# Performance work log

Hardware: AMD Instinct MI355X
Metric: run time of the kernel (lower is better)

Reference implementation:

```python
import jax, jax.numpy as jnp
import numpy as np

N_HEADS = 16


def setup_inputs() -> dict:
    key = jax.random.key(0)
    k1, k2, k3 = jax.random.split(key, 3)
    B, T, D = 2, 2048, 1024
    x = jax.random.normal(k1, (B, T, D), dtype=jnp.float32)
    w_qkv = jax.random.normal(k2, (3 * D, D), dtype=jnp.float32) * 0.02
    w_proj = jax.random.normal(k3, (D, D), dtype=jnp.float32) * (0.02 / np.sqrt(24.0))
    return {"x": x, "w_qkv": w_qkv, "w_proj": w_proj}


def reference(x, w_qkv, w_proj):
    B, T, D = x.shape
    H = N_HEADS
    dh = D // H
    # qkv linear (no bias): x @ w_qkv.T -> [B, T, 3D]
    qkv = jnp.einsum('btd,ed->bte', x, w_qkv)
    q, k, v = jnp.split(qkv, 3, axis=-1)
    q = q.reshape(B, T, H, dh)
    k = k.reshape(B, T, H, dh)
    v = v.reshape(B, T, H, dh)
    # attention with materialized scores [B, H, T, S]
    scores = jnp.einsum('bthd,bshd->bhts', q, k) / jnp.sqrt(jnp.asarray(dh, x.dtype))
    attn = jax.nn.softmax(scores.astype(jnp.float32), axis=-1).astype(x.dtype)
    out = jnp.einsum('bhts,bshd->bthd', attn, v).reshape(B, T, D)
    # output projection (no bias)
    return jnp.einsum('btd,ed->bte', out, w_proj)
```

## Files before the change

kernel.cpp:

```cpp
#include <hip/hip_runtime.h>


typedef __attribute__((ext_vector_type(8))) short s8v;
typedef __attribute__((ext_vector_type(8))) unsigned short us8;
typedef __attribute__((ext_vector_type(4))) unsigned short us4;
typedef __attribute__((ext_vector_type(4))) float f4v;
typedef __attribute__((ext_vector_type(16))) float f16v;
typedef __attribute__((ext_vector_type(4))) unsigned u4v;

__device__ __forceinline__ unsigned short f2b(float f) {
    unsigned u = __builtin_bit_cast(unsigned, f);
    u += 0x7FFFu + ((u >> 16) & 1u);
    return (unsigned short)(u >> 16);
}
__device__ __forceinline__ unsigned packtrunc(float a, float b, unsigned sel) {
    unsigned r;
    asm("v_perm_b32 %0, %1, %2, %3"
        : "=v"(r)
        : "v"(__builtin_bit_cast(unsigned, b)), "v"(__builtin_bit_cast(unsigned, a)), "s"(sel));
    return r;
}

#if __has_builtin(__builtin_amdgcn_exp2f)
#define EXP2F(x) __builtin_amdgcn_exp2f(x)
#else
#define EXP2F(x) exp2f(x)
#endif

#define QSCALE 0.18033688011112042f

__global__ __launch_bounds__(256) void cvt_all(const float* __restrict__ x,
                                               const float* __restrict__ wq,
                                               const float* __restrict__ wp,
                                               unsigned short* __restrict__ xb,
                                               unsigned short* __restrict__ wqb,
                                               unsigned short* __restrict__ wpb) {
    const int nx = 4096 * 1024 / 4, nq = 3072 * 1024 / 4;
    int i = blockIdx.x * 256 + threadIdx.x;
    const float* s;
    unsigned short* d;
    int j;
    if (i < nx)           { s = x;  d = xb;  j = i; }
    else if (i < nx + nq) { s = wq; d = wqb; j = i - nx; }
    else                  { s = wp; d = wpb; j = i - nx - nq; }
    float4 v = ((const float4*)s)[j];
    ushort4 o;
    o.x = f2b(v.x); o.y = f2b(v.y); o.z = f2b(v.z); o.w = f2b(v.w);
    ((ushort4*)d)[j] = o;
}

#define GLD_LDS16(g, l)                                                                        \
    __builtin_amdgcn_global_load_lds((const __attribute__((address_space(1))) unsigned*)(g),   \
                                     (__attribute__((address_space(3))) unsigned*)(l), 16, 0, 0)

__global__ __launch_bounds__(256, 4) void gemm_qkv(const unsigned short* __restrict__ A,
                                                   const unsigned short* __restrict__ B,
                                                   unsigned short* __restrict__ qkvb) {
    __shared__ unsigned short As[128][64];
    __shared__ unsigned short Bs[128][64];
    const int tid = threadIdx.x;
    const int l = tid & 63, w = tid >> 6;
    const int quad = l >> 4, ln = l & 15;
    const int m0 = blockIdx.y * 128, n0 = blockIdx.x * 128;
    const int wm = (w >> 1) * 64, wn = (w & 1) * 64;

    const f4v fz = {0.f, 0.f, 0.f, 0.f};
    f4v acc[4][4];
#pragma unroll
    for (int i = 0; i < 4; ++i)
#pragma unroll
        for (int j = 0; j < 4; ++j) acc[i][j] = fz;

    const int srow = tid >> 3, sc8 = tid & 7;
    const int gcol = ((sc8 ^ (srow & 7)) << 3);
    const int koff0 = ((quad ^ (ln & 7)) << 3);
    const int koff1 = (((4 + quad) ^ (ln & 7)) << 3);

    const unsigned short* pa = A + (size_t)(m0 + srow) * 1024 + gcol;
    const unsigned short* pb = B + (size_t)(n0 + srow) * 1024 + gcol;

    for (int k0 = 0; k0 < 1024; k0 += 64) {
#pragma unroll
        for (int b = 0; b < 4; ++b) {
            GLD_LDS16(pa + (size_t)32 * b * 1024 + k0, &As[srow + 32 * b][sc8 * 8]);
            GLD_LDS16(pb + (size_t)32 * b * 1024 + k0, &Bs[srow + 32 * b][sc8 * 8]);
        }
        __syncthreads();
#pragma unroll
        for (int ks = 0; ks < 2; ++ks) {
            const int ko = ks ? koff1 : koff0;
            s8v af[4], bf[4];
#pragma unroll
            for (int mt = 0; mt < 4; ++mt) af[mt] = *(const s8v*)&As[wm + mt * 16 + ln][ko];
#pragma unroll
            for (int nt = 0; nt < 4; ++nt) bf[nt] = *(const s8v*)&Bs[wn + nt * 16 + ln][ko];
#pragma unroll
            for (int mt = 0; mt < 4; ++mt)
#pragma unroll
                for (int nt = 0; nt < 4; ++nt)
                    acc[mt][nt] = __builtin_amdgcn_mfma_f32_16x16x32_bf16(af[mt], bf[nt], acc[mt][nt], 0, 0, 0);
        }
        __syncthreads();
    }

#pragma unroll
    for (int mt = 0; mt < 4; ++mt)
#pragma unroll
        for (int nt = 0; nt < 4; ++nt) {
            const int col = n0 + wn + nt * 16 + ln;
            const int row = m0 + wm + mt * 16 + quad * 4;
            const float sc = (col < 1024) ? QSCALE : 1.0f;
#pragma unroll
            for (int r = 0; r < 4; ++r)
                qkvb[(size_t)(row + r) * 3072 + col] = f2b(acc[mt][nt][r] * sc);
        }
}

__global__ __launch_bounds__(256, 4) void gemm_proj(const unsigned short* __restrict__ A,
                                                    const unsigned short* __restrict__ B,
                                                    float* __restrict__ C) {
    __shared__ unsigned short As[64][64];
    __shared__ unsigned short Bs[64][64];
    const int tid = threadIdx.x;
    const int l = tid & 63, w = tid >> 6;
    const int quad = l >> 4, ln = l & 15;
    const int m0 = blockIdx.y * 64, n0 = blockIdx.x * 64;
    const int wm = (w >> 1) * 32, wn = (w & 1) * 32;

    const f4v fz = {0.f, 0.f, 0.f, 0.f};
    f4v acc[2][2];
#pragma unroll
    for (int i = 0; i < 2; ++i)
#pragma unroll
        for (int j = 0; j < 2; ++j) acc[i][j] = fz;

    const int srow = tid >> 3, sc8 = tid & 7;
    const int gcol = ((sc8 ^ (srow & 7)) << 3);
    const int koff0 = ((quad ^ (ln & 7)) << 3);
    const int koff1 = (((4 + quad) ^ (ln & 7)) << 3);

    for (int k0 = 0; k0 < 1024; k0 += 64) {
#pragma unroll
        for (int b = 0; b < 2; ++b) {
            GLD_LDS16(A + (size_t)(m0 + srow + 32 * b) * 1024 + k0 + gcol, &As[srow + 32 * b][sc8 * 8]);
            GLD_LDS16(B + (size_t)(n0 + srow + 32 * b) * 1024 + k0 + gcol, &Bs[srow + 32 * b][sc8 * 8]);
        }
        __syncthreads();
#pragma unroll
        for (int ks = 0; ks < 2; ++ks) {
            const int ko = ks ? koff1 : koff0;
            s8v af[2], bf[2];
#pragma unroll
            for (int mt = 0; mt < 2; ++mt) af[mt] = *(const s8v*)&As[wm + mt * 16 + ln][ko];
#pragma unroll
            for (int nt = 0; nt < 2; ++nt) bf[nt] = *(const s8v*)&Bs[wn + nt * 16 + ln][ko];
#pragma unroll
            for (int mt = 0; mt < 2; ++mt)
#pragma unroll
                for (int nt = 0; nt < 2; ++nt)
                    acc[mt][nt] = __builtin_amdgcn_mfma_f32_16x16x32_bf16(af[mt], bf[nt], acc[mt][nt], 0, 0, 0);
        }
        __syncthreads();
    }

#pragma unroll
    for (int mt = 0; mt < 2; ++mt)
#pragma unroll
        for (int nt = 0; nt < 2; ++nt) {
            const int row = m0 + wm + mt * 16 + quad * 4;
            const int col = n0 + wn + nt * 16 + ln;
#pragma unroll
            for (int r = 0; r < 4; ++r) C[(size_t)(row + r) * 1024 + col] = acc[mt][nt][r];
        }
}

__global__ __launch_bounds__(256, 4) void attn_split(const unsigned short* __restrict__ qkvb,
                                                     float* __restrict__ opart,
                                                     float* __restrict__ lpart) {
    __shared__ unsigned short Ks[2][64][76];
    __shared__ unsigned short Vt[2][64][76];

    const int tid = threadIdx.x;
    const int l = tid & 63, w = tid >> 6;
    const int m31 = l & 31, h2 = l >> 5;
    const int qw = w * 32;
    const int t0 = blockIdx.x * 128;
    const int hh = blockIdx.y;
    const int bb = blockIdx.z >> 1, sp = blockIdx.z & 1;
    const size_t rowbase = (size_t)bb * 2048;
    const int sbase = sp * 1024;
    const unsigned sel = 0x07060302u;

#pragma unroll
    for (int it = 0; it < 4; ++it) {
        const int idx = tid + it * 256;
        const int qr = idx >> 3, qc = (idx & 7) * 8;
        unsigned short* dst = (qr < 64) ? &Ks[0][qr][qc] : &Ks[1][qr - 64][qc];
        *(us8*)dst = *(const us8*)(qkvb + (rowbase + t0 + qr) * 3072 + hh * 64 + qc);
    }
    __syncthreads();
    s8v qf[4];
    {
        const int qrow = qw + m31;
#pragma unroll
        for (int k4 = 0; k4 < 4; ++k4)
            qf[k4] = (qrow < 64) ? *(const s8v*)&Ks[0][qrow][k4 * 16 + h2 * 8]
                                 : *(const s8v*)&Ks[1][qrow - 64][k4 * 16 + h2 * 8];
    }
    __syncthreads();

    const int r0 = tid >> 3, c0 = (tid & 7) * 8;
    const int va = tid >> 4, vc = tid & 15;

    f16v zz;
#pragma unroll
    for (int i = 0; i < 16; ++i) zz[i] = 0.f;
    f16v oacc[2];
    oacc[0] = zz; oacc[1] = zz;
    float lsum = 0.f;

    us8 kreg0 = *(const us8*)(qkvb + (rowbase + sbase + r0) * 3072 + 1024 + hh * 64 + c0);
    us8 kreg1 = *(const us8*)(qkvb + (rowbase + sbase + r0 + 32) * 3072 + 1024 + hh * 64 + c0);
    us4 vreg[4];
#pragma unroll
    for (int j = 0; j < 4; ++j)
        vreg[j] = *(const us4*)(qkvb + (rowbase + sbase + 4 * va + j) * 3072 + 2048 + hh * 64 + 4 * vc);
    *(us8*)&Ks[0][r0][c0] = kreg0;
    *(us8*)&Ks[0][r0 + 32][c0] = kreg1;
#pragma unroll
    for (int dd = 0; dd < 4; ++dd) {
        unsigned lo = (unsigned)vreg[0][dd] | ((unsigned)vreg[1][dd] << 16);
        unsigned hi = (unsigned)vreg[2][dd] | ((unsigned)vreg[3][dd] << 16);
        uint2 pk2; pk2.x = lo; pk2.y = hi;
        *(uint2*)&Vt[0][4 * vc + dd][4 * va] = pk2;
    }

    for (int i = 0; i < 16; ++i) {
        const int cur = i & 1;
        __syncthreads();

        if (i + 1 < 16) {
            const size_t sn = rowbase + sbase + (i + 1) * 64;
            kreg0 = *(const us8*)(qkvb + (sn + r0) * 3072 + 1024 + hh * 64 + c0);
            kreg1 = *(const us8*)(qkvb + (sn + r0 + 32) * 3072 + 1024 + hh * 64 + c0);
#pragma unroll
            for (int j = 0; j < 4; ++j)
                vreg[j] = *(const us4*)(qkvb + (sn + 4 * va + j) * 3072 + 2048 + hh * 64 + 4 * vc);
        }

#pragma unroll
        for (int st = 0; st < 2; ++st) {
            f16v sacc = zz;
            __builtin_amdgcn_s_setprio(1);
#pragma unroll
            for (int k4 = 0; k4 < 4; ++k4) {
                s8v kf = *(const s8v*)&Ks[cur][st * 32 + m31][k4 * 16 + h2 * 8];
                sacc = __builtin_amdgcn_mfma_f32_32x32x16_bf16(kf, qf[k4], sacc, 0, 0, 0);
            }
            __builtin_amdgcn_s_setprio(0);
            unsigned wv[4][2];
#pragma unroll
            for (int g = 0; g < 4; ++g) {
                float p0 = EXP2F(sacc[g * 4 + 0]);
                float p1 = EXP2F(sacc[g * 4 + 1]);
                float p2 = EXP2F(sacc[g * 4 + 2]);
                float p3 = EXP2F(sacc[g * 4 + 3]);
                lsum += (p0 + p1) + (p2 + p3);
                wv[g][0] = packtrunc(p0, p1, sel);
                wv[g][1] = packtrunc(p2, p3, sel);
            }
            __builtin_amdgcn_s_setprio(1);
#pragma unroll
            for (int e = 0; e < 2; ++e) {
                auto ra = __builtin_amdgcn_permlane32_swap(wv[2 * e][0], wv[2 * e + 1][0], false, false);
                auto rb = __builtin_amdgcn_permlane32_swap(wv[2 * e][1], wv[2 * e + 1][1], false, false);
                u4v t;
                t[0] = ra[0]; t[1] = rb[0];
                t[2] = ra[1]; t[3] = rb[1];
                s8v pf = __builtin_bit_cast(s8v, t);
                const int k2 = 2 * st + e;
#pragma unroll
                for (int nt = 0; nt < 2; ++nt) {
                    s8v vfr = *(const s8v*)&Vt[cur][nt * 32 + m31][k2 * 16 + h2 * 8];
                    oacc[nt] = __builtin_amdgcn_mfma_f32_32x32x16_bf16(pf, vfr, oacc[nt], 0, 0, 0);
                }
            }
            __builtin_amdgcn_s_setprio(0);
        }

        if (i + 1 < 16) {
            *(us8*)&Ks[1 - cur][r0][c0] = kreg0;
            *(us8*)&Ks[1 - cur][r0 + 32][c0] = kreg1;
#pragma unroll
            for (int dd = 0; dd < 4; ++dd) {
                unsigned lo = (unsigned)vreg[0][dd] | ((unsigned)vreg[1][dd] << 16);
                unsigned hi = (unsigned)vreg[2][dd] | ((unsigned)vreg[3][dd] << 16);
                uint2 pk2; pk2.x = lo; pk2.y = hi;
                *(uint2*)&Vt[1 - cur][4 * vc + dd][4 * va] = pk2;
            }
        }
    }

    lsum += __shfl_xor(lsum, 32, 64);
    if (h2 == 0)
        lpart[((size_t)sp * 4096 + rowbase + t0 + qw + m31) * 16 + hh] = lsum;

    float* op = opart + (size_t)sp * 4096 * 1024;
#pragma unroll
    for (int nt = 0; nt < 2; ++nt)
#pragma unroll
        for (int g = 0; g < 4; ++g)
#pragma unroll
            for (int r = 0; r < 4; ++r) {
                const int qrow = 8 * g + 4 * h2 + r;
                op[(rowbase + t0 + qw + qrow) * 1024 + hh * 64 + nt * 32 + m31] = oacc[nt][g * 4 + r];
            }
}

__global__ __launch_bounds__(256) void attn_combine(const float* __restrict__ opart,
                                                    const float* __restrict__ lpart,
                                                    unsigned short* __restrict__ attnb) {
    const int idx = blockIdx.x * 256 + threadIdx.x;
    const int r = idx >> 8, c4 = (idx & 255) << 2, h = c4 >> 6;
    const size_t fi = (size_t)r * 256 + (c4 >> 2);
    float4 o0 = ((const float4*)opart)[fi];
    float4 o1 = ((const float4*)(opart + (size_t)4096 * 1024))[fi];
    float ls = lpart[(size_t)r * 16 + h] + lpart[((size_t)4096 + r) * 16 + h];
    float s = 1.001955f / ls;
    ushort4 o;
    o.x = f2b((o0.x + o1.x) * s);
    o.y = f2b((o0.y + o1.y) * s);
    o.z = f2b((o0.z + o1.z) * s);
    o.w = f2b((o0.w + o1.w) * s);
    ((ushort4*)attnb)[fi] = o;
}

__global__ __launch_bounds__(256) void attn_mfma(const unsigned short* __restrict__ qkvb,
                                                 unsigned short* __restrict__ attnb) {
    __shared__ unsigned short Ks[2][64][76];
    __shared__ unsigned short Vt[2][64][76];
    __shared__ float lred[128];

    const int tid = threadIdx.x;
    const int l = tid & 63, w = tid >> 6;
    const int m31 = l & 31, h2 = l >> 5;
    const int qw = w * 32;
    const int t0 = blockIdx.x * 128;
    const int hh = blockIdx.y, bb = blockIdx.z;
    const size_t rowbase = (size_t)bb * 2048;
    const unsigned sel = 0x07060302u;

#pragma unroll
    for (int it = 0; it < 4; ++it) {
        const int idx = tid + it * 256;
        const int qr = idx >> 3, qc = (idx & 7) * 8;
        unsigned short* dst = (qr < 64) ? &Ks[0][qr][qc] : &Ks[1][qr - 64][qc];
        *(us8*)dst = *(const us8*)(qkvb + (rowbase + t0 + qr) * 3072 + hh * 64 + qc);
    }
    __syncthreads();
    s8v qf[4];
    {
        const int qrow = qw + m31;
#pragma unroll
        for (int k4 = 0; k4 < 4; ++k4)
            qf[k4] = (qrow < 64) ? *(const s8v*)&Ks[0][qrow][k4 * 16 + h2 * 8]
                                 : *(const s8v*)&Ks[1][qrow - 64][k4 * 16 + h2 * 8];
    }
    __syncthreads();

    const int r0 = tid >> 3, c0 = (tid & 7) * 8;
    const int va = tid >> 4, vc = tid & 15;

    f16v zz;
#pragma unroll
    for (int i = 0; i < 16; ++i) zz[i] = 0.f;
    f16v oacc[2];
    oacc[0] = zz; oacc[1] = zz;
    float lsum = 0.f;

    us8 kreg0 = *(const us8*)(qkvb + (rowbase + r0) * 3072 + 1024 + hh * 64 + c0);
    us8 kreg1 = *(const us8*)(qkvb + (rowbase + r0 + 32) * 3072 + 1024 + hh * 64 + c0);
    us4 vreg[4];
#pragma unroll
    for (int j = 0; j < 4; ++j)
        vreg[j] = *(const us4*)(qkvb + (rowbase + 4 * va + j) * 3072 + 2048 + hh * 64 + 4 * vc);
    *(us8*)&Ks[0][r0][c0] = kreg0;
    *(us8*)&Ks[0][r0 + 32][c0] = kreg1;
#pragma unroll
    for (int dd = 0; dd < 4; ++dd) {
        unsigned lo = (unsigned)vreg[0][dd] | ((unsigned)vreg[1][dd] << 16);
        unsigned hi = (unsigned)vreg[2][dd] | ((unsigned)vreg[3][dd] << 16);
        uint2 pk2; pk2.x = lo; pk2.y = hi;
        *(uint2*)&Vt[0][4 * vc + dd][4 * va] = pk2;
    }

    for (int i = 0; i < 32; ++i) {
        const int cur = i & 1;
        __syncthreads();

        if (i + 1 < 32) {
            const int sn = (i + 1) * 64;
            kreg0 = *(const us8*)(qkvb + (rowbase + sn + r0) * 3072 + 1024 + hh * 64 + c0);
            kreg1 = *(const us8*)(qkvb + (rowbase + sn + r0 + 32) * 3072 + 1024 + hh * 64 + c0);
#pragma unroll
            for (int j = 0; j < 4; ++j)
                vreg[j] = *(const us4*)(qkvb + (rowbase + sn + 4 * va + j) * 3072 + 2048 + hh * 64 + 4 * vc);
        }

        f16v sacc[2];
        sacc[0] = zz; sacc[1] = zz;
#pragma unroll
        for (int k4 = 0; k4 < 4; ++k4) {
#pragma unroll
            for (int st = 0; st < 2; ++st) {
                s8v kf = *(const s8v*)&Ks[cur][st * 32 + m31][k4 * 16 + h2 * 8];
                sacc[st] = __builtin_amdgcn_mfma_f32_32x32x16_bf16(kf, qf[k4], sacc[st], 0, 0, 0);
            }
        }

        unsigned wv[2][4][2];
#pragma unroll
        for (int st = 0; st < 2; ++st)
#pragma unroll
            for (int g = 0; g < 4; ++g) {
                float p0 = EXP2F(sacc[st][g * 4 + 0]);
                float p1 = EXP2F(sacc[st][g * 4 + 1]);
                float p2 = EXP2F(sacc[st][g * 4 + 2]);
                float p3 = EXP2F(sacc[st][g * 4 + 3]);
                lsum += (p0 + p1) + (p2 + p3);
                wv[st][g][0] = packtrunc(p0, p1, sel);
                wv[st][g][1] = packtrunc(p2, p3, sel);
            }

        s8v pf[4];
#pragma unroll
        for (int st = 0; st < 2; ++st)
#pragma unroll
            for (int e = 0; e < 2; ++e) {
                auto ra = __builtin_amdgcn_permlane32_swap(wv[st][2 * e][0], wv[st][2 * e + 1][0], false, false);
                auto rb = __builtin_amdgcn_permlane32_swap(wv[st][2 * e][1], wv[st][2 * e + 1][1], false, false);
                u4v t;
                t[0] = ra[0]; t[1] = rb[0];
                t[2] = ra[1]; t[3] = rb[1];
                pf[2 * st + e] = __builtin_bit_cast(s8v, t);
            }

#pragma unroll
        for (int k2 = 0; k2 < 4; ++k2) {
#pragma unroll
            for (int nt = 0; nt < 2; ++nt) {
                s8v vfr = *(const s8v*)&Vt[cur][nt * 32 + m31][k2 * 16 + h2 * 8];
                oacc[nt] = __builtin_amdgcn_mfma_f32_32x32x16_bf16(pf[k2], vfr, oacc[nt], 0, 0, 0);
            }
        }

        if (i + 1 < 32) {
            *(us8*)&Ks[1 - cur][r0][c0] = kreg0;
            *(us8*)&Ks[1 - cur][r0 + 32][c0] = kreg1;
#pragma unroll
            for (int dd = 0; dd < 4; ++dd) {
                unsigned lo = (unsigned)vreg[0][dd] | ((unsigned)vreg[1][dd] << 16);
                unsigned hi = (unsigned)vreg[2][dd] | ((unsigned)vreg[3][dd] << 16);
                uint2 pk2; pk2.x = lo; pk2.y = hi;
                *(uint2*)&Vt[1 - cur][4 * vc + dd][4 * va] = pk2;
            }
        }
    }

    lsum += __shfl_xor(lsum, 32, 64);
    lred[qw + m31] = lsum;
    float inv[16];
#pragma unroll
    for (int g = 0; g < 4; ++g)
#pragma unroll
        for (int r = 0; r < 4; ++r)
            inv[g * 4 + r] = 1.001955f / lred[qw + 8 * g + 4 * h2 + r];

#pragma unroll
    for (int nt = 0; nt < 2; ++nt)
#pragma unroll
        for (int g = 0; g < 4; ++g)
#pragma unroll
            for (int r = 0; r < 4; ++r) {
                const int qrow = 8 * g + 4 * h2 + r;
                float o = oacc[nt][g * 4 + r] * inv[g * 4 + r];
                attnb[(rowbase + t0 + qw + qrow) * 1024 + hh * 64 + nt * 32 + m31] = f2b(o);
            }
}

extern "C" void kernel_launch(void* const* d_in, const int* in_sizes, int n_in,
                              void* d_out, int out_size, void* d_ws, size_t ws_size,
                              hipStream_t stream) {
    const float* x      = (const float*)d_in[0];
    const float* w_qkv  = (const float*)d_in[1];
    const float* w_proj = (const float*)d_in[2];
    float* out = (float*)d_out;

    char* p = (char*)d_ws;
    unsigned short* xb    = (unsigned short*)p;  p += (size_t)4096 * 1024 * 2;
    unsigned short* wqb   = (unsigned short*)p;  p += (size_t)3072 * 1024 * 2;
    unsigned short* wpb   = (unsigned short*)p;  p += (size_t)1024 * 1024 * 2;
    unsigned short* qkvb  = (unsigned short*)p;  p += (size_t)4096 * 3072 * 2;
    unsigned short* attnb = (unsigned short*)p;  p += (size_t)4096 * 1024 * 2;
    float* opart = (float*)p;  p += (size_t)2 * 4096 * 1024 * 4;
    float* lpart = (float*)p;  p += (size_t)2 * 4096 * 16 * 4;
    const size_t need = (size_t)(p - (char*)d_ws);

    cvt_all<<<8192, 256, 0, stream>>>(x, w_qkv, w_proj, xb, wqb, wpb);

    gemm_qkv<<<dim3(3072 / 128, 4096 / 128), 256, 0, stream>>>(xb, wqb, qkvb);

    if (ws_size >= need) {
        attn_split<<<dim3(2048 / 128, 16, 4), 256, 0, stream>>>(qkvb, opart, lpart);
        attn_combine<<<4096, 256, 0, stream>>>(opart, lpart, attnb);
    } else {
        attn_mfma<<<dim3(2048 / 128, 16, 2), 256, 0, stream>>>(qkvb, attnb);
    }

    gemm_proj<<<dim3(1024 / 64, 4096 / 64), 256, 0, stream>>>(attnb, wpb, out);
}
```

Baseline: 176.8 us.

## Fuse all stages into one cooperative persistent kernel with grid syncs

Replaces the five separate launches (convert, QKV GEMM, split attention, combine, projection GEMM) with a single cooperative kernel of 1024 blocks that runs each stage in turn, separated by grid.sync(). The aim is to remove per-launch overhead and the idle gaps between kernels. The cost is grid-wide barriers and fixed block-to-work mappings: the QKV GEMM uses only 768 of the 1024 blocks, and every stage is limited to 1024 resident blocks. The cooperative path is taken only when the stream is not being captured, and the old multi-kernel path remains as a fallback.

```diff
diff --git a/kernel.cpp b/kernel.cpp
--- a/kernel.cpp
+++ b/kernel.cpp
@@ -1,4 +1,7 @@
 #include <hip/hip_runtime.h>
+#include <hip/hip_cooperative_groups.h>
+
+namespace cg = cooperative_groups;
 
 
 typedef __attribute__((ext_vector_type(8))) short s8v;
@@ -28,6 +31,325 @@
 #endif
 
 #define QSCALE 0.18033688011112042f
+
+#define GLD_LDS16(g, l)                                                                        \
+    __builtin_amdgcn_global_load_lds((const __attribute__((address_space(1))) unsigned*)(g),   \
+                                     (__attribute__((address_space(3))) unsigned*)(l), 16, 0, 0)
+
+typedef unsigned short row64_t[64];
+typedef unsigned short kvbuf_t[64][76];
+
+__global__ __launch_bounds__(256, 4) void mha_mega(const float* __restrict__ x,
+                                                   const float* __restrict__ wq,
+                                                   const float* __restrict__ wp,
+                                                   unsigned short* __restrict__ xb,
+                                                   unsigned short* __restrict__ wqb,
+                                                   unsigned short* __restrict__ wpb,
+                                                   unsigned short* __restrict__ qkvb,
+                                                   float* __restrict__ opart,
+                                                   float* __restrict__ lpart,
+                                                   float* __restrict__ out) {
+    __shared__ __align__(16) unsigned char smem[38912];
+    const int tid = threadIdx.x;
+    const int bid = blockIdx.x;
+    cg::grid_group grid = cg::this_grid();
+
+    {
+        const int nx = 4096 * 1024 / 4, nq = 3072 * 1024 / 4;
+#pragma unroll
+        for (int it = 0; it < 8; ++it) {
+            const int i = it * 262144 + bid * 256 + tid;
+            const float* s;
+            unsigned short* d;
+            int j;
+            if (i < nx)           { s = x;  d = xb;  j = i; }
+            else if (i < nx + nq) { s = wq; d = wqb; j = i - nx; }
+            else                  { s = wp; d = wpb; j = i - nx - nq; }
+            float4 v = ((const float4*)s)[j];
+            ushort4 o;
+            o.x = f2b(v.x); o.y = f2b(v.y); o.z = f2b(v.z); o.w = f2b(v.w);
+            ((ushort4*)d)[j] = o;
+        }
+    }
+    grid.sync();
+
+    if (bid < 768) {
+        row64_t* As = (row64_t*)smem;
+        row64_t* Bs = (row64_t*)(smem + 128 * 64 * 2);
+        const int l = tid & 63, w = tid >> 6;
+        const int quad = l >> 4, ln = l & 15;
+        const int m0 = (bid / 24) * 128, n0 = (bid % 24) * 128;
+        const int wm = (w >> 1) * 64, wn = (w & 1) * 64;
+
+        const f4v fz = {0.f, 0.f, 0.f, 0.f};
+        f4v acc[4][4];
+#pragma unroll
+        for (int i = 0; i < 4; ++i)
+#pragma unroll
+            for (int j = 0; j < 4; ++j) acc[i][j] = fz;
+
+        const int srow = tid >> 3, sc8 = tid & 7;
+        const int gcol = ((sc8 ^ (srow & 7)) << 3);
+        const int koff0 = ((quad ^ (ln & 7)) << 3);
+        const int koff1 = (((4 + quad) ^ (ln & 7)) << 3);
+
+        const unsigned short* pa = xb + (size_t)(m0 + srow) * 1024 + gcol;
+        const unsigned short* pb = wqb + (size_t)(n0 + srow) * 1024 + gcol;
+
+        for (int k0 = 0; k0 < 1024; k0 += 64) {
+#pragma unroll
+            for (int b = 0; b < 4; ++b) {
+                GLD_LDS16(pa + (size_t)32 * b * 1024 + k0, &As[srow + 32 * b][sc8 * 8]);
+                GLD_LDS16(pb + (size_t)32 * b * 1024 + k0, &Bs[srow + 32 * b][sc8 * 8]);
+            }
+            __syncthreads();
+#pragma unroll
+            for (int ks = 0; ks < 2; ++ks) {
+                const int ko = ks ? koff1 : koff0;
+                s8v af[4], bf[4];
+#pragma unroll
+                for (int mt = 0; mt < 4; ++mt) af[mt] = *(const s8v*)&As[wm + mt * 16 + ln][ko];
+#pragma unroll
+                for (int nt = 0; nt < 4; ++nt) bf[nt] = *(const s8v*)&Bs[wn + nt * 16 + ln][ko];
+#pragma unroll
+                for (int mt = 0; mt < 4; ++mt)
+#pragma unroll
+                    for (int nt = 0; nt < 4; ++nt)
+                        acc[mt][nt] = __builtin_amdgcn_mfma_f32_16x16x32_bf16(af[mt], bf[nt], acc[mt][nt], 0, 0, 0);
+            }
+            __syncthreads();
+        }
+
+#pragma unroll
+        for (int mt = 0; mt < 4; ++mt)
+#pragma unroll
+            for (int nt = 0; nt < 4; ++nt) {
+                const int col = n0 + wn + nt * 16 + ln;
+                const int row = m0 + wm + mt * 16 + quad * 4;
+                const float sc = (col < 1024) ? QSCALE : 1.0f;
+#pragma unroll
+                for (int r = 0; r < 4; ++r)
+                    qkvb[(size_t)(row + r) * 3072 + col] = f2b(acc[mt][nt][r] * sc);
+            }
+    }
+    grid.sync();
+
+    {
+        kvbuf_t* Ks = (kvbuf_t*)smem;
+        kvbuf_t* Vt = (kvbuf_t*)(smem + 2 * sizeof(kvbuf_t));
+        const int l = tid & 63, w = tid >> 6;
+        const int m31 = l & 31, h2 = l >> 5;
+        const int qw = w * 32;
+        const int t0 = (bid & 15) * 128;
+        const int hh = (bid >> 4) & 15;
+        const int spz = bid >> 8;
+        const int bb = spz >> 1, sp = spz & 1;
+        const size_t rowbase = (size_t)bb * 2048;
+        const int sbase = sp * 1024;
+        const unsigned sel = 0x07060302u;
+
+#pragma unroll
+        for (int it = 0; it < 4; ++it) {
+            const int idx = tid + it * 256;
+            const int qr = idx >> 3, qc = (idx & 7) * 8;
+            unsigned short* dst = (qr < 64) ? &Ks[0][qr][qc] : &Ks[1][qr - 64][qc];
+            *(us8*)dst = *(const us8*)(qkvb + (rowbase + t0 + qr) * 3072 + hh * 64 + qc);
+        }
+        __syncthreads();
+        s8v qf[4];
+        {
+            const int qrow = qw + m31;
+#pragma unroll
+            for (int k4 = 0; k4 < 4; ++k4)
+                qf[k4] = (qrow < 64) ? *(const s8v*)&Ks[0][qrow][k4 * 16 + h2 * 8]
+                                     : *(const s8v*)&Ks[1][qrow - 64][k4 * 16 + h2 * 8];
+        }
+        __syncthreads();
+
+        const int r0 = tid >> 3, c0 = (tid & 7) * 8;
+        const int va = tid >> 4, vc = tid & 15;
+
+        f16v zz;
+#pragma unroll
+        for (int i = 0; i < 16; ++i) zz[i] = 0.f;
+        f16v oacc[2];
+        oacc[0] = zz; oacc[1] = zz;
+        float lsum = 0.f;
+
+        us8 kreg0 = *(const us8*)(qkvb + (rowbase + sbase + r0) * 3072 + 1024 + hh * 64 + c0);
+        us8 kreg1 = *(const us8*)(qkvb + (rowbase + sbase + r0 + 32) * 3072 + 1024 + hh * 64 + c0);
+        us4 vreg[4];
+#pragma unroll
+        for (int j = 0; j < 4; ++j)
+            vreg[j] = *(const us4*)(qkvb + (rowbase + sbase + 4 * va + j) * 3072 + 2048 + hh * 64 + 4 * vc);
+        *(us8*)&Ks[0][r0][c0] = kreg0;
+        *(us8*)&Ks[0][r0 + 32][c0] = kreg1;
+#pragma unroll
+        for (int dd = 0; dd < 4; ++dd) {
+            unsigned lo = (unsigned)vreg[0][dd] | ((unsigned)vreg[1][dd] << 16);
+            unsigned hi = (unsigned)vreg[2][dd] | ((unsigned)vreg[3][dd] << 16);
+            uint2 pk2; pk2.x = lo; pk2.y = hi;
+            *(uint2*)&Vt[0][4 * vc + dd][4 * va] = pk2;
+        }
+
+        for (int i = 0; i < 16; ++i) {
+            const int cur = i & 1;
+            __syncthreads();
+
+            if (i + 1 < 16) {
+                const size_t sn = rowbase + sbase + (i + 1) * 64;
+                kreg0 = *(const us8*)(qkvb + (sn + r0) * 3072 + 1024 + hh * 64 + c0);
+                kreg1 = *(const us8*)(qkvb + (sn + r0 + 32) * 3072 + 1024 + hh * 64 + c0);
+#pragma unroll
+                for (int j = 0; j < 4; ++j)
+                    vreg[j] = *(const us4*)(qkvb + (sn + 4 * va + j) * 3072 + 2048 + hh * 64 + 4 * vc);
+            }
+
+#pragma unroll
+            for (int st = 0; st < 2; ++st) {
+                f16v sacc = zz;
+                __builtin_amdgcn_s_setprio(1);
+#pragma unroll
+                for (int k4 = 0; k4 < 4; ++k4) {
+                    s8v kf = *(const s8v*)&Ks[cur][st * 32 + m31][k4 * 16 + h2 * 8];
+                    sacc = __builtin_amdgcn_mfma_f32_32x32x16_bf16(kf, qf[k4], sacc, 0, 0, 0);
+                }
+                __builtin_amdgcn_s_setprio(0);
+                unsigned wv[4][2];
+#pragma unroll
+                for (int g = 0; g < 4; ++g) {
+                    float p0 = EXP2F(sacc[g * 4 + 0]);
+                    float p1 = EXP2F(sacc[g * 4 + 1]);
+                    float p2 = EXP2F(sacc[g * 4 + 2]);
+                    float p3 = EXP2F(sacc[g * 4 + 3]);
+                    lsum += (p0 + p1) + (p2 + p3);
+                    wv[g][0] = packtrunc(p0, p1, sel);
+                    wv[g][1] = packtrunc(p2, p3, sel);
+                }
+                __builtin_amdgcn_s_setprio(1);
+#pragma unroll
+                for (int e = 0; e < 2; ++e) {
+                    auto ra = __builtin_amdgcn_permlane32_swap(wv[2 * e][0], wv[2 * e + 1][0], false, false);
+                    auto rb = __builtin_amdgcn_permlane32_swap(wv[2 * e][1], wv[2 * e + 1][1], false, false);
+                    u4v t;
+                    t[0] = ra[0]; t[1] = rb[0];
+                    t[2] = ra[1]; t[3] = rb[1];
+                    s8v pf = __builtin_bit_cast(s8v, t);
+                    const int k2 = 2 * st + e;
+#pragma unroll
+                    for (int nt = 0; nt < 2; ++nt) {
+                        s8v vfr = *(const s8v*)&Vt[cur][nt * 32 + m31][k2 * 16 + h2 * 8];
+                        oacc[nt] = __builtin_amdgcn_mfma_f32_32x32x16_bf16(pf, vfr, oacc[nt], 0, 0, 0);
+                    }
+                }
+                __builtin_amdgcn_s_setprio(0);
+            }
+
+            if (i + 1 < 16) {
+                *(us8*)&Ks[1 - cur][r0][c0] = kreg0;
+                *(us8*)&Ks[1 - cur][r0 + 32][c0] = kreg1;
+#pragma unroll
+                for (int dd = 0; dd < 4; ++dd) {
+                    unsigned lo = (unsigned)vreg[0][dd] | ((unsigned)vreg[1][dd] << 16);
+                    unsigned hi = (unsigned)vreg[2][dd] | ((unsigned)vreg[3][dd] << 16);
+                    uint2 pk2; pk2.x = lo; pk2.y = hi;
+                    *(uint2*)&Vt[1 - cur][4 * vc + dd][4 * va] = pk2;
+                }
+            }
+        }
+
+        lsum += __shfl_xor(lsum, 32, 64);
+        if (h2 == 0)
+            lpart[((size_t)sp * 4096 + rowbase + t0 + qw + m31) * 16 + hh] = lsum;
+
+        float* op = opart + (size_t)sp * 4096 * 1024;
+#pragma unroll
+        for (int nt = 0; nt < 2; ++nt)
+#pragma unroll
+            for (int g = 0; g < 4; ++g)
+#pragma unroll
+                for (int r = 0; r < 4; ++r) {
+                    const int qrow = 8 * g + 4 * h2 + r;
+                    op[(rowbase + t0 + qw + qrow) * 1024 + hh * 64 + nt * 32 + m31] = oacc[nt][g * 4 + r];
+                }
+    }
+    grid.sync();
+
+    {
+#pragma unroll
+        for (int it = 0; it < 4; ++it) {
+            const int idx = it * 262144 + bid * 256 + tid;
+            const int r = idx >> 8, c4 = (idx & 255) << 2, h = c4 >> 6;
+            const size_t fi = (size_t)r * 256 + (c4 >> 2);
+            float4 o0 = ((const float4*)opart)[fi];
+            float4 o1 = ((const float4*)(opart + (size_t)4096 * 1024))[fi];
+            float ls = lpart[(size_t)r * 16 + h] + lpart[((size_t)4096 + r) * 16 + h];
+            float s = 1.001955f / ls;
+            ushort4 o;
+            o.x = f2b((o0.x + o1.x) * s);
+            o.y = f2b((o0.y + o1.y) * s);
+            o.z = f2b((o0.z + o1.z) * s);
+            o.w = f2b((o0.w + o1.w) * s);
+            ((ushort4*)xb)[fi] = o;
+        }
+    }
+    grid.sync();
+
+    {
+        row64_t* As = (row64_t*)smem;
+        row64_t* Bs = (row64_t*)(smem + 64 * 64 * 2);
+        const int l = tid & 63, w = tid >> 6;
+        const int quad = l >> 4, ln = l & 15;
+        const int m0 = (bid >> 4) * 64, n0 = (bid & 15) * 64;
+        const int wm = (w >> 1) * 32, wn = (w & 1) * 32;
+
+        const f4v fz = {0.f, 0.f, 0.f, 0.f};
+        f4v acc[2][2];
+#pragma unroll
+        for (int i = 0; i < 2; ++i)
+#pragma unroll
+            for (int j = 0; j < 2; ++j) acc[i][j] = fz;
+
+        const int srow = tid >> 3, sc8 = tid & 7;
+        const int gcol = ((sc8 ^ (srow & 7)) << 3);
+        const int koff0 = ((quad ^ (ln & 7)) << 3);
+        const int koff1 = (((4 + quad) ^ (ln & 7)) << 3);
+
+        for (int k0 = 0; k0 < 1024; k0 += 64) {
+#pragma unroll
+            for (int b = 0; b < 2; ++b) {
+                GLD_LDS16(xb + (size_t)(m0 + srow + 32 * b) * 1024 + k0 + gcol, &As[srow + 32 * b][sc8 * 8]);
+                GLD_LDS16(wpb + (size_t)(n0 + srow + 32 * b) * 1024 + k0 + gcol, &Bs[srow + 32 * b][sc8 * 8]);
+            }
+            __syncthreads();
+#pragma unroll
+            for (int ks = 0; ks < 2; ++ks) {
+                const int ko = ks ? koff1 : koff0;
+                s8v af[2], bf[2];
+#pragma unroll
+                for (int mt = 0; mt < 2; ++mt) af[mt] = *(const s8v*)&As[wm + mt * 16 + ln][ko];
+#pragma unroll
+                for (int nt = 0; nt < 2; ++nt) bf[nt] = *(const s8v*)&Bs[wn + nt * 16 + ln][ko];
+#pragma unroll
+                for (int mt = 0; mt < 2; ++mt)
+#pragma unroll
+                    for (int nt = 0; nt < 2; ++nt)
+                        acc[mt][nt] = __builtin_amdgcn_mfma_f32_16x16x32_bf16(af[mt], bf[nt], acc[mt][nt], 0, 0, 0);
+            }
+            __syncthreads();
+        }
+
+#pragma unroll
+        for (int mt = 0; mt < 2; ++mt)
+#pragma unroll
+            for (int nt = 0; nt < 2; ++nt) {
+                const int row = m0 + wm + mt * 16 + quad * 4;
+                const int col = n0 + wn + nt * 16 + ln;
+#pragma unroll
+                for (int r = 0; r < 4; ++r) out[(size_t)(row + r) * 1024 + col] = acc[mt][nt][r];
+            }
+    }
+}
 
 __global__ __launch_bounds__(256) void cvt_all(const float* __restrict__ x,
                                                const float* __restrict__ wq,
@@ -49,10 +371,6 @@
     ((ushort4*)d)[j] = o;
 }
 
-#define GLD_LDS16(g, l)                                                                        \
-    __builtin_amdgcn_global_load_lds((const __attribute__((address_space(1))) unsigned*)(g),   \
-                                     (__attribute__((address_space(3))) unsigned*)(l), 16, 0, 0)
-
 __global__ __launch_bounds__(256, 4) void gemm_qkv(const unsigned short* __restrict__ A,
                                                    const unsigned short* __restrict__ B,
                                                    unsigned short* __restrict__ qkvb) {
@@ -506,16 +824,31 @@
     float* lpart = (float*)p;  p += (size_t)2 * 4096 * 16 * 4;
     const size_t need = (size_t)(p - (char*)d_ws);
 
-    cvt_all<<<8192, 256, 0, stream>>>(x, w_qkv, w_proj, xb, wqb, wpb);
-
-    gemm_qkv<<<dim3(3072 / 128, 4096 / 128), 256, 0, stream>>>(xb, wqb, qkvb);
-
     if (ws_size >= need) {
+        hipStreamCaptureStatus cap = hipStreamCaptureStatusActive;
+        if (hipStreamIsCapturing(stream, &cap) != hipSuccess)
+            cap = hipStreamCaptureStatusActive;
+
+        if (cap == hipStreamCaptureStatusNone) {
+            void* args[] = {(void*)&x, (void*)&w_qkv, (void*)&w_proj,
+                            (void*)&xb, (void*)&wqb, (void*)&wpb,
+                            (void*)&qkvb, (void*)&opart, (void*)&lpart, (void*)&out};
+            hipError_t e = hipLaunchCooperativeKernel((void*)mha_mega, dim3(1024), dim3(256),
+                                                      args, 0, stream);
+            if (e == hipSuccess) return;
+            (void)hipGetLastError();
+        }
+
+        cvt_all<<<8192, 256, 0, stream>>>(x, w_qkv, w_proj, xb, wqb, wpb);
+        gemm_qkv<<<dim3(3072 / 128, 4096 / 128), 256, 0, stream>>>(xb, wqb, qkvb);
         attn_split<<<dim3(2048 / 128, 16, 4), 256, 0, stream>>>(qkvb, opart, lpart);
         attn_combine<<<4096, 256, 0, stream>>>(opart, lpart, attnb);
-    } else {
-        attn_mfma<<<dim3(2048 / 128, 16, 2), 256, 0, stream>>>(qkvb, attnb);
-    }
-
+        gemm_proj<<<dim3(1024 / 64, 4096 / 64), 256, 0, stream>>>(attnb, wpb, out);
+        return;
+    }
+
+    cvt_all<<<8192, 256, 0, stream>>>(x, w_qkv, w_proj, xb, wqb, wpb);
+    gemm_qkv<<<dim3(3072 / 128, 4096 / 128), 256, 0, stream>>>(xb, wqb, qkvb);
+    attn_mfma<<<dim3(2048 / 128, 16, 2), 256, 0, stream>>>(qkvb, attnb);
     gemm_proj<<<dim3(1024 / 64, 4096 / 64), 256, 0, stream>>>(attnb, wpb, out);
 }
```

Result: no change. 180.4 us (+2.0%).
